# Optimization experiments

Hardware: AMD Instinct MI355X
Metric: run time of the kernel (lower is better)

Reference implementation:

```python
import jax, jax.numpy as jnp
import numpy as np

N, E, F_IN, H = 100000, 500000, 1433, 32


def setup_inputs() -> dict:
    key = jax.random.key(0)
    ks = jax.random.split(key, 8)
    return {
        "x": jax.random.normal(ks[0], (N, F_IN), jnp.float32),
        "edge_index": jax.random.randint(ks[1], (2, E), 0, N, dtype=jnp.int32),
        "W1l": jax.random.normal(ks[2], (H, F_IN), jnp.float32) * 0.02,
        "b1l": jnp.zeros((H,), jnp.float32),
        "W1r": jax.random.normal(ks[3], (H, F_IN), jnp.float32) * 0.02,
        "W2l": jax.random.normal(ks[4], (H, H), jnp.float32) * 0.1,
        "b2l": jnp.zeros((H,), jnp.float32),
        "W2r": jax.random.normal(ks[5], (H, H), jnp.float32) * 0.1,
    }


def _sage_conv(x, src, tgt, Wl, bl, Wr, n_nodes):
    # PyG SAGEConv (mean aggr): out = lin_l(mean_{j->i} x_j) + lin_r(x_i)
    msg_sum = jax.ops.segment_sum(x[src], tgt, num_segments=n_nodes)  # [N, d]
    cnt = jax.ops.segment_sum(jnp.ones((src.shape[0],), x.dtype), tgt,
                              num_segments=n_nodes)                  # [N]
    agg = msg_sum / jnp.maximum(cnt, 1.0)[:, None]  # isolated nodes -> 0
    return agg @ Wl.T + bl + x @ Wr.T


def reference(x, edge_index, W1l, b1l, W1r, W2l, b2l, W2r):
    src, tgt = edge_index[0], edge_index[1]
    n = x.shape[0]
    h = _sage_conv(x, src, tgt, W1l, b1l, W1r, n)   # [N, 32]
    h = _sage_conv(h, src, tgt, W2l, b2l, W2r, n)   # [N, 32]
    h = jax.nn.relu(h)
    # dropout is identity in eval mode (training=False)
    return jax.nn.log_softmax(h, axis=1)
```

## Files before the change

kernel.cpp:

```cpp
#include <hip/hip_runtime.h>
#include <hip/hip_bf16.h>


typedef __attribute__((ext_vector_type(8))) __bf16 bf16x8;
typedef __attribute__((ext_vector_type(4))) float f32x4;

constexpr int K1 = 1433;
constexpr int KP1 = 1536;
constexpr int BK = 32;
constexpr int NS = 45;
constexpr int BM = 128;

__device__ __forceinline__ void gload_lds16(const void* g, void* l) {
  __builtin_amdgcn_global_load_lds(
      reinterpret_cast<const __attribute__((address_space(1))) void*>(
          reinterpret_cast<uintptr_t>(g)),
      reinterpret_cast<__attribute__((address_space(3))) void*>(
          reinterpret_cast<uintptr_t>(l)),
      16, 0, 0);
}

__device__ __forceinline__ bf16x8 cvt8(const float4 lo, const float4 hi) {
  bf16x8 r;
  r[0] = (__bf16)lo.x; r[1] = (__bf16)lo.y;
  r[2] = (__bf16)lo.z; r[3] = (__bf16)lo.w;
  r[4] = (__bf16)hi.x; r[5] = (__bf16)hi.y;
  r[6] = (__bf16)hi.z; r[7] = (__bf16)hi.w;
  return r;
}

__global__ __launch_bounds__(256) void conv_w(const float* __restrict__ Wl,
                                              const float* __restrict__ Wr,
                                              __bf16* __restrict__ out, int K,
                                              int KP) {
  const int t = blockIdx.x * 256 + threadIdx.x;
  if (t >= 64 * KP) return;
  const int c = t / KP, k = t - c * KP;
  float v = 0.0f;
  if (k < K) v = (c < 32) ? Wl[(long)c * K + k] : Wr[(long)(c - 32) * K + k];
  out[t] = (__bf16)v;
}

__global__ __launch_bounds__(256) void gemm_big(const float* __restrict__ X,
                                                const __bf16* __restrict__ WB,
                                                float* __restrict__ Y,
                                                int Nrows) {
  __shared__ float ldsA[2][BM][BK];
  __shared__ __bf16 ldsB[2][64][BK];
  const int tid = threadIdx.x;
  const int w = tid >> 6, l = tid & 63;
  const int lr = l & 15, lg = l >> 4;
  const int row0 = blockIdx.x * BM;

  const int aRowIn = (l >> 3);
  const int aChunk = (l & 7) ^ aRowIn;
  long aRow[4];
#pragma unroll
  for (int i = 0; i < 4; ++i) {
    long r = (long)row0 + w * 32 + i * 8 + aRowIn;
    if (r >= Nrows) r = Nrows - 1;
    aRow[i] = r;
  }
  const float* const pAmax = X + (size_t)Nrows * K1 - 4;
  const int bRow = w * 16 + (l >> 2);
  const int bChunk = (l & 3) ^ ((l >> 3) & 3);
  const __bf16* const pB0 = WB + (long)bRow * KP1 + bChunk * 8;

  auto stage = [&](int s, int buf) {
    const int k0 = s * BK;
#pragma unroll
    for (int i = 0; i < 4; ++i) {
      const float* g = X + aRow[i] * K1 + k0 + aChunk * 4;
      if (g > pAmax) g = pAmax;
      gload_lds16(g, &ldsA[buf][w * 32 + i * 8][0]);
    }
    gload_lds16(pB0 + k0, &ldsB[buf][w * 16][0]);
  };

  f32x4 acc[2][4];
#pragma unroll
  for (int t = 0; t < 2; ++t)
#pragma unroll
    for (int j = 0; j < 4; ++j) acc[t][j] = (f32x4){0.f, 0.f, 0.f, 0.f};

  const int swzA = lr & 7;
  const int swzB = (lr >> 1) & 3;

  stage(0, 0);
#pragma unroll 1
  for (int s = 0; s < NS; ++s) {
    const int buf = s & 1;
    if (s + 1 < NS) {
      stage(s + 1, buf ^ 1);
      asm volatile("s_waitcnt vmcnt(5)" ::: "memory");
    } else {
      asm volatile("s_waitcnt vmcnt(0)" ::: "memory");
    }
    __builtin_amdgcn_s_barrier();
    __builtin_amdgcn_sched_barrier(0);
    bf16x8 bfrag[4];
#pragma unroll
    for (int ct = 0; ct < 4; ++ct) {
      const int br = ct * 16 + lr;
      bfrag[ct] = *reinterpret_cast<const bf16x8*>(
          &ldsB[buf][br][(lg ^ swzB) * 8]);
    }
#pragma unroll
    for (int t = 0; t < 2; ++t) {
      const int fr = w * 32 + t * 16 + lr;
      const float4 u = *reinterpret_cast<const float4*>(
          &ldsA[buf][fr][((lg * 2 + 0) ^ swzA) * 4]);
      const float4 v = *reinterpret_cast<const float4*>(
          &ldsA[buf][fr][((lg * 2 + 1) ^ swzA) * 4]);
      const bf16x8 af = cvt8(u, v);
#pragma unroll
      for (int ct = 0; ct < 4; ++ct)
        acc[t][ct] =
            __builtin_amdgcn_mfma_f32_16x16x32_bf16(af, bfrag[ct], acc[t][ct], 0, 0, 0);
    }
    __builtin_amdgcn_sched_barrier(0);
    __builtin_amdgcn_s_barrier();
  }

#pragma unroll
  for (int t = 0; t < 2; ++t) {
#pragma unroll
    for (int j = 0; j < 4; ++j) {
      const long R = (long)row0 + w * 32 + t * 16 + lg * 4 + j;
      if (R < Nrows) {
#pragma unroll
        for (int ct = 0; ct < 4; ++ct)
          Y[R * 64 + ct * 16 + lr] = acc[t][ct][j];
      }
    }
  }
}

__global__ __launch_bounds__(256) void gemm_small(const float* __restrict__ X,
                                                  const __bf16* __restrict__ WB,
                                                  float* __restrict__ Y,
                                                  int Nrows) {
  const int tid = threadIdx.x;
  const int w = tid >> 6, l = tid & 63;
  const int lr = l & 15, lg = l >> 4;
  const long rowbase = (long)blockIdx.x * 64 + (long)w * 16;
  long r0 = rowbase + lr;
  if (r0 >= Nrows) r0 = Nrows - 1;
  const float* px = X + r0 * 32 + lg * 8;
  const __bf16* pw = WB + lr * 32 + lg * 8;

  const float4 lo = *reinterpret_cast<const float4*>(px);
  const float4 hi = *reinterpret_cast<const float4*>(px + 4);
  const bf16x8 af = cvt8(lo, hi);
  f32x4 acc[4];
#pragma unroll
  for (int j = 0; j < 4; ++j) acc[j] = (f32x4){0.f, 0.f, 0.f, 0.f};
#pragma unroll
  for (int t = 0; t < 4; ++t) {
    const bf16x8 bf = *reinterpret_cast<const bf16x8*>(pw + t * 16 * 32);
    acc[t] = __builtin_amdgcn_mfma_f32_16x16x32_bf16(af, bf, acc[t], 0, 0, 0);
  }
#pragma unroll
  for (int j = 0; j < 4; ++j) {
    const long R = rowbase + lg * 4 + j;
    if (R < Nrows) {
#pragma unroll
      for (int ct = 0; ct < 4; ++ct) Y[R * 64 + ct * 16 + lr] = acc[ct][j];
    }
  }
}


__global__ __launch_bounds__(256) void hist_deg(const int* __restrict__ ei,
                                                int* __restrict__ deg, int E) {
  const int e = blockIdx.x * 256 + threadIdx.x;
  if (e < E) atomicAdd(&deg[ei[E + e]], 1);
}

__global__ __launch_bounds__(256) void scan_tilesum(const int* __restrict__ deg,
                                                    int* __restrict__ tileSum,
                                                    int n) {
  __shared__ int s[256];
  const int b = blockIdx.x, t = threadIdx.x;
  const int base = b * 2048 + t * 8;
  int v = 0;
#pragma unroll
  for (int j = 0; j < 8; ++j) {
    const int i = base + j;
    if (i < n) v += deg[i];
  }
  s[t] = v;
  __syncthreads();
  for (int d = 128; d > 0; d >>= 1) {
    if (t < d) s[t] += s[t + d];
    __syncthreads();
  }
  if (t == 0) tileSum[b] = s[0];
}

__global__ __launch_bounds__(64) void scan_tileoff(const int* __restrict__ tileSum,
                                                   int* __restrict__ tileOff,
                                                   int nT) {
  const int l = threadIdx.x;
  const int v = (l < nT) ? tileSum[l] : 0;
  int inc = v;
#pragma unroll
  for (int d = 1; d < 64; d <<= 1) {
    const int o = __shfl_up(inc, d);
    if (l >= d) inc += o;
  }
  if (l < nT) tileOff[l] = inc - v;
}

__global__ __launch_bounds__(256) void scan_offsets(const int* __restrict__ deg,
                                                    const int* __restrict__ tileOff,
                                                    int* __restrict__ off, int n) {
  __shared__ int warpTot[4];
  const int b = blockIdx.x, t = threadIdx.x;
  const int base = b * 2048 + t * 8;
  int v[8];
  int s = 0;
#pragma unroll
  for (int j = 0; j < 8; ++j) {
    const int i = base + j;
    v[j] = (i < n) ? deg[i] : 0;
    s += v[j];
  }
  const int l = t & 63, w = t >> 6;
  int inc = s;
#pragma unroll
  for (int d = 1; d < 64; d <<= 1) {
    const int o = __shfl_up(inc, d);
    if (l >= d) inc += o;
  }
  if (l == 63) warpTot[w] = inc;
  __syncthreads();
  int wo = 0;
  for (int k = 0; k < w; ++k) wo += warpTot[k];
  int ex = wo + (inc - s) + tileOff[b];
#pragma unroll
  for (int j = 0; j < 8; ++j) {
    const int i = base + j;
    if (i < n) {
      off[i] = ex;
      ex += v[j];
    }
  }
}

__global__ __launch_bounds__(256) void scatter_src(const int* __restrict__ ei,
                                                   const int* __restrict__ off,
                                                   int* __restrict__ fill,
                                                   int* __restrict__ ssrc,
                                                   int E) {
  const int e = blockIdx.x * 256 + threadIdx.x;
  if (e < E) {
    const int t = ei[E + e];
    const int p = off[t] + atomicAdd(&fill[t], 1);
    ssrc[p] = ei[e];
  }
}

template <int FINAL>
__global__ __launch_bounds__(256) void agg_fused(
    const int* __restrict__ off, const int* __restrict__ deg,
    const int* __restrict__ ssrc, const float* __restrict__ Y,
    const float* __restrict__ bias, float* __restrict__ out, int N) {
  const int t = blockIdx.x * 256 + threadIdx.x;
  const int i = t >> 5, c = t & 31;
  if (i >= N) return;
  const int st = off[i], d = deg[i];
  float acc = 0.0f;
  int e = 0;
  for (; e + 4 <= d; e += 4) {
    const int s0 = ssrc[st + e + 0];
    const int s1 = ssrc[st + e + 1];
    const int s2 = ssrc[st + e + 2];
    const int s3 = ssrc[st + e + 3];
    acc += Y[(long)s0 * 64 + c] + Y[(long)s1 * 64 + c] +
           Y[(long)s2 * 64 + c] + Y[(long)s3 * 64 + c];
  }
  for (; e < d; ++e) acc += Y[(long)ssrc[st + e] * 64 + c];
  const float mean = acc / fmaxf((float)d, 1.0f);
  float v = mean + bias[c] + Y[(long)i * 64 + 32 + c];
  if (FINAL) {
    v = fmaxf(v, 0.0f);
    float m = v;
#pragma unroll
    for (int dd = 16; dd >= 1; dd >>= 1) m = fmaxf(m, __shfl_xor(m, dd));
    const float ex = __expf(v - m);
    float s = ex;
#pragma unroll
    for (int dd = 16; dd >= 1; dd >>= 1) s += __shfl_xor(s, dd);
    out[(long)i * 32 + c] = (v - m) - __logf(s);
  } else {
    out[(long)i * 32 + c] = v;
  }
}

extern "C" void kernel_launch(void* const* d_in, const int* in_sizes, int n_in,
                              void* d_out, int out_size, void* d_ws,
                              size_t ws_size, hipStream_t stream) {
  const float* x = (const float*)d_in[0];
  const int* ei = (const int*)d_in[1];
  const float* W1l = (const float*)d_in[2];
  const float* b1l = (const float*)d_in[3];
  const float* W1r = (const float*)d_in[4];
  const float* W2l = (const float*)d_in[5];
  const float* b2l = (const float*)d_in[6];
  const float* W2r = (const float*)d_in[7];
  float* out = (float*)d_out;

  const int N = in_sizes[0] / K1;
  const int E = in_sizes[1] / 2;
  const int nTiles = (N + 2047) / 2048;

  char* ws = (char*)d_ws;
  size_t o = 0;
  auto alloc = [&](size_t bytes) {
    void* p = ws + o;
    o += (bytes + 255) & ~(size_t)255;
    return p;
  };
  float* ycomb = (float*)alloc((size_t)N * 64 * 4);
  float* h = (float*)alloc((size_t)N * 32 * 4);
  __bf16* wb1 = (__bf16*)alloc((size_t)64 * KP1 * 2);
  __bf16* wb2 = (__bf16*)alloc((size_t)64 * 32 * 2);
  int* deg = (int*)alloc((size_t)N * 4);
  int* off = (int*)alloc((size_t)N * 4);
  int* fill = (int*)alloc((size_t)N * 4);
  int* ssrc = (int*)alloc((size_t)E * 4);
  int* tileSum = (int*)alloc(64 * 4);
  int* tileOff = (int*)alloc(64 * 4);

  conv_w<<<(64 * KP1 + 255) / 256, 256, 0, stream>>>(W1l, W1r, wb1, K1, KP1);
  conv_w<<<(64 * 32 + 255) / 256, 256, 0, stream>>>(W2l, W2r, wb2, 32, 32);
  (void)hipMemsetAsync(deg, 0, (size_t)N * 4, stream);
  (void)hipMemsetAsync(fill, 0, (size_t)N * 4, stream);
  hist_deg<<<(E + 255) / 256, 256, 0, stream>>>(ei, deg, E);
  scan_tilesum<<<nTiles, 256, 0, stream>>>(deg, tileSum, N);
  scan_tileoff<<<1, 64, 0, stream>>>(tileSum, tileOff, nTiles);
  scan_offsets<<<nTiles, 256, 0, stream>>>(deg, tileOff, off, N);
  scatter_src<<<(E + 255) / 256, 256, 0, stream>>>(ei, off, fill, ssrc, E);

  gemm_big<<<(N + BM - 1) / BM, 256, 0, stream>>>(x, wb1, ycomb, N);
  agg_fused<0><<<(N * 32 + 255) / 256, 256, 0, stream>>>(off, deg, ssrc, ycomb,
                                                         b1l, h, N);
  gemm_small<<<(N + 63) / 64, 256, 0, stream>>>(h, wb2, ycomb, N);
  agg_fused<1><<<(N * 32 + 255) / 256, 256, 0, stream>>>(off, deg, ssrc, ycomb,
                                                         b2l, out, N);
}
```

Measured before the change: 300.8 us.

## Retile big GEMM to 32-row blocks with 256-deep K stages

Reorganizes the first-layer GEMM to use 32-row tiles with 256-wide K stages (6 stages instead of 45), each wave loading whole contiguous row segments and the four waves splitting the tile 2x2 over rows and output columns. Intended to cut per-stage barrier/loop overhead and improve load contiguity while raising block count. In exchange LDS use grows to about 128 KB per block, limiting occupancy to one block per CU, and the weight matrix is reloaded by four times as many blocks.

```diff
diff --git a/kernel.cpp b/kernel.cpp
--- a/kernel.cpp
+++ b/kernel.cpp
@@ -7,9 +7,9 @@
 
 constexpr int K1 = 1433;
 constexpr int KP1 = 1536;
-constexpr int BK = 32;
-constexpr int NS = 45;
-constexpr int BM = 128;
+constexpr int BK2 = 256;
+constexpr int NS2 = 6;
+constexpr int BM2 = 32;
 
 __device__ __forceinline__ void gload_lds16(const void* g, void* l) {
   __builtin_amdgcn_global_load_lds(
@@ -45,93 +45,91 @@
                                                 const __bf16* __restrict__ WB,
                                                 float* __restrict__ Y,
                                                 int Nrows) {
-  __shared__ float ldsA[2][BM][BK];
-  __shared__ __bf16 ldsB[2][64][BK];
+  __shared__ float ldsA[2][BM2][BK2];
+  __shared__ __bf16 ldsB[2][64][BK2];
   const int tid = threadIdx.x;
   const int w = tid >> 6, l = tid & 63;
   const int lr = l & 15, lg = l >> 4;
-  const int row0 = blockIdx.x * BM;
-
-  const int aRowIn = (l >> 3);
-  const int aChunk = (l & 7) ^ aRowIn;
-  long aRow[4];
-#pragma unroll
-  for (int i = 0; i < 4; ++i) {
-    long r = (long)row0 + w * 32 + i * 8 + aRowIn;
+  const int wr = w >> 1, wc = w & 1;
+  const int row0 = blockIdx.x * BM2;
+
+  const float* pA[8];
+#pragma unroll
+  for (int i = 0; i < 8; ++i) {
+    long r = (long)row0 + w * 8 + i;
     if (r >= Nrows) r = Nrows - 1;
-    aRow[i] = r;
+    pA[i] = X + r * (long)K1 + ((l ^ i) << 2);
   }
   const float* const pAmax = X + (size_t)Nrows * K1 - 4;
-  const int bRow = w * 16 + (l >> 2);
-  const int bChunk = (l & 3) ^ ((l >> 3) & 3);
-  const __bf16* const pB0 = WB + (long)bRow * KP1 + bChunk * 8;
+  const __bf16* pB[8];
+#pragma unroll
+  for (int j = 0; j < 8; ++j) {
+    const int J = w * 8 + j;
+    const int brow = 2 * J + (l >> 5);
+    pB[j] = WB + (long)brow * KP1 + (((l & 31) ^ (brow & 7)) << 3);
+  }
 
   auto stage = [&](int s, int buf) {
-    const int k0 = s * BK;
-#pragma unroll
-    for (int i = 0; i < 4; ++i) {
-      const float* g = X + aRow[i] * K1 + k0 + aChunk * 4;
+    const int k0 = s * BK2;
+#pragma unroll
+    for (int i = 0; i < 8; ++i) {
+      const float* g = pA[i] + k0;
       if (g > pAmax) g = pAmax;
-      gload_lds16(g, &ldsA[buf][w * 32 + i * 8][0]);
-    }
-    gload_lds16(pB0 + k0, &ldsB[buf][w * 16][0]);
+      gload_lds16(g, &ldsA[buf][w * 8 + i][0]);
+    }
+#pragma unroll
+    for (int j = 0; j < 8; ++j) {
+      gload_lds16(pB[j] + k0, &ldsB[buf][2 * (w * 8 + j)][0]);
+    }
   };
 
-  f32x4 acc[2][4];
-#pragma unroll
-  for (int t = 0; t < 2; ++t)
-#pragma unroll
-    for (int j = 0; j < 4; ++j) acc[t][j] = (f32x4){0.f, 0.f, 0.f, 0.f};
-
-  const int swzA = lr & 7;
-  const int swzB = (lr >> 1) & 3;
+  f32x4 acc[2];
+#pragma unroll
+  for (int ct = 0; ct < 2; ++ct) acc[ct] = (f32x4){0.f, 0.f, 0.f, 0.f};
+
+  const int swz = (lr & 7) << 4;
 
   stage(0, 0);
 #pragma unroll 1
-  for (int s = 0; s < NS; ++s) {
+  for (int s = 0; s < NS2; ++s) {
     const int buf = s & 1;
-    if (s + 1 < NS) {
+    if (s + 1 < NS2) {
       stage(s + 1, buf ^ 1);
-      asm volatile("s_waitcnt vmcnt(5)" ::: "memory");
+      asm volatile("s_waitcnt vmcnt(16)" ::: "memory");
     } else {
       asm volatile("s_waitcnt vmcnt(0)" ::: "memory");
     }
     __builtin_amdgcn_s_barrier();
     __builtin_amdgcn_sched_barrier(0);
-    bf16x8 bfrag[4];
-#pragma unroll
-    for (int ct = 0; ct < 4; ++ct) {
-      const int br = ct * 16 + lr;
-      bfrag[ct] = *reinterpret_cast<const bf16x8*>(
-          &ldsB[buf][br][(lg ^ swzB) * 8]);
-    }
-#pragma unroll
-    for (int t = 0; t < 2; ++t) {
-      const int fr = w * 32 + t * 16 + lr;
-      const float4 u = *reinterpret_cast<const float4*>(
-          &ldsA[buf][fr][((lg * 2 + 0) ^ swzA) * 4]);
-      const float4 v = *reinterpret_cast<const float4*>(
-          &ldsA[buf][fr][((lg * 2 + 1) ^ swzA) * 4]);
+#pragma unroll
+    for (int ks = 0; ks < 8; ++ks) {
+      const char* arow = (const char*)&ldsA[buf][wr * 16 + lr][0];
+      const int b0 = ks * 128 + lg * 32;
+      const float4 u = *reinterpret_cast<const float4*>(arow + (b0 ^ swz));
+      const float4 v =
+          *reinterpret_cast<const float4*>(arow + ((b0 + 16) ^ swz));
       const bf16x8 af = cvt8(u, v);
 #pragma unroll
-      for (int ct = 0; ct < 4; ++ct)
-        acc[t][ct] =
-            __builtin_amdgcn_mfma_f32_16x16x32_bf16(af, bfrag[ct], acc[t][ct], 0, 0, 0);
+      for (int ct = 0; ct < 2; ++ct) {
+        const char* bp =
+            (const char*)&ldsB[buf][wc * 32 + ct * 16 + lr][0];
+        const bf16x8 bf = *reinterpret_cast<const bf16x8*>(
+            bp + ((ks * 64 + lg * 16) ^ swz));
+        acc[ct] =
+            __builtin_amdgcn_mfma_f32_16x16x32_bf16(af, bf, acc[ct], 0, 0, 0);
+      }
     }
     __builtin_amdgcn_sched_barrier(0);
     __builtin_amdgcn_s_barrier();
   }
 
 #pragma unroll
-  for (int t = 0; t < 2; ++t) {
-#pragma unroll
-    for (int j = 0; j < 4; ++j) {
-      const long R = (long)row0 + w * 32 + t * 16 + lg * 4 + j;
-      if (R < Nrows) {
-#pragma unroll
-        for (int ct = 0; ct < 4; ++ct)
-          Y[R * 64 + ct * 16 + lr] = acc[t][ct][j];
-      }
+  for (int j = 0; j < 4; ++j) {
+    const long R = (long)row0 + wr * 16 + lg * 4 + j;
+    if (R < Nrows) {
+#pragma unroll
+      for (int ct = 0; ct < 2; ++ct)
+        Y[R * 64 + wc * 32 + ct * 16 + lr] = acc[ct][j];
     }
   }
 }
@@ -343,7 +341,7 @@
   scan_offsets<<<nTiles, 256, 0, stream>>>(deg, tileOff, off, N);
   scatter_src<<<(E + 255) / 256, 256, 0, stream>>>(ei, off, fill, ssrc, E);
 
-  gemm_big<<<(N + BM - 1) / BM, 256, 0, stream>>>(x, wb1, ycomb, N);
+  gemm_big<<<(N + BM2 - 1) / BM2, 256, 0, stream>>>(x, wb1, ycomb, N);
   agg_fused<0><<<(N * 32 + 255) / 256, 256, 0, stream>>>(off, deg, ssrc, ycomb,
                                                          b1l, h, N);
   gemm_small<<<(N + 63) / 64, 256, 0, stream>>>(h, wb2, ycomb, N);
```

Result: slower. 323.6 us (+7.6%).

## Fuse layer-1 aggregation with layer-2 GEMM and merge small setup kernels

Applied to the files above, without the earlier changes.

The first mean-aggregation now writes its 64-node tile of h as bf16 into shared memory, and the small 32x64 MFMA GEMM runs in the same kernel. This removes the h round trip through global memory and the separate gemm_small launch. The kernel also merges the two weight-conversion kernels, folds the tile-offset scan into scan_offsets, and clears deg and fill with a single memset, cutting several launches. In exchange each block processes its 8 nodes per row group serially, which may reduce the memory-level parallelism of the gather. A second Y buffer is also needed.

```diff
diff --git a/kernel.cpp b/kernel.cpp
--- a/kernel.cpp
+++ b/kernel.cpp
@@ -29,16 +29,27 @@
   return r;
 }
 
-__global__ __launch_bounds__(256) void conv_w(const float* __restrict__ Wl,
-                                              const float* __restrict__ Wr,
-                                              __bf16* __restrict__ out, int K,
-                                              int KP) {
+__global__ __launch_bounds__(256) void conv_w2(const float* __restrict__ W1l,
+                                               const float* __restrict__ W1r,
+                                               const float* __restrict__ W2l,
+                                               const float* __restrict__ W2r,
+                                               __bf16* __restrict__ wb1,
+                                               __bf16* __restrict__ wb2) {
   const int t = blockIdx.x * 256 + threadIdx.x;
-  if (t >= 64 * KP) return;
-  const int c = t / KP, k = t - c * KP;
-  float v = 0.0f;
-  if (k < K) v = (c < 32) ? Wl[(long)c * K + k] : Wr[(long)(c - 32) * K + k];
-  out[t] = (__bf16)v;
+  if (t < 64 * KP1) {
+    const int c = t / KP1, k = t - c * KP1;
+    float v = 0.0f;
+    if (k < K1)
+      v = (c < 32) ? W1l[(long)c * K1 + k] : W1r[(long)(c - 32) * K1 + k];
+    wb1[t] = (__bf16)v;
+  } else {
+    const int u = t - 64 * KP1;
+    if (u < 64 * 32) {
+      const int c = u >> 5, k = u & 31;
+      const float v = (c < 32) ? W2l[c * 32 + k] : W2r[(c - 32) * 32 + k];
+      wb2[u] = (__bf16)v;
+    }
+  }
 }
 
 __global__ __launch_bounds__(256) void gemm_big(const float* __restrict__ X,
@@ -136,40 +147,6 @@
   }
 }
 
-__global__ __launch_bounds__(256) void gemm_small(const float* __restrict__ X,
-                                                  const __bf16* __restrict__ WB,
-                                                  float* __restrict__ Y,
-                                                  int Nrows) {
-  const int tid = threadIdx.x;
-  const int w = tid >> 6, l = tid & 63;
-  const int lr = l & 15, lg = l >> 4;
-  const long rowbase = (long)blockIdx.x * 64 + (long)w * 16;
-  long r0 = rowbase + lr;
-  if (r0 >= Nrows) r0 = Nrows - 1;
-  const float* px = X + r0 * 32 + lg * 8;
-  const __bf16* pw = WB + lr * 32 + lg * 8;
-
-  const float4 lo = *reinterpret_cast<const float4*>(px);
-  const float4 hi = *reinterpret_cast<const float4*>(px + 4);
-  const bf16x8 af = cvt8(lo, hi);
-  f32x4 acc[4];
-#pragma unroll
-  for (int j = 0; j < 4; ++j) acc[j] = (f32x4){0.f, 0.f, 0.f, 0.f};
-#pragma unroll
-  for (int t = 0; t < 4; ++t) {
-    const bf16x8 bf = *reinterpret_cast<const bf16x8*>(pw + t * 16 * 32);
-    acc[t] = __builtin_amdgcn_mfma_f32_16x16x32_bf16(af, bf, acc[t], 0, 0, 0);
-  }
-#pragma unroll
-  for (int j = 0; j < 4; ++j) {
-    const long R = rowbase + lg * 4 + j;
-    if (R < Nrows) {
-#pragma unroll
-      for (int ct = 0; ct < 4; ++ct) Y[R * 64 + ct * 16 + lr] = acc[ct][j];
-    }
-  }
-}
-
 
 __global__ __launch_bounds__(256) void hist_deg(const int* __restrict__ ei,
                                                 int* __restrict__ deg, int E) {
@@ -198,25 +175,19 @@
   if (t == 0) tileSum[b] = s[0];
 }
 
-__global__ __launch_bounds__(64) void scan_tileoff(const int* __restrict__ tileSum,
-                                                   int* __restrict__ tileOff,
-                                                   int nT) {
-  const int l = threadIdx.x;
-  const int v = (l < nT) ? tileSum[l] : 0;
-  int inc = v;
-#pragma unroll
-  for (int d = 1; d < 64; d <<= 1) {
-    const int o = __shfl_up(inc, d);
-    if (l >= d) inc += o;
-  }
-  if (l < nT) tileOff[l] = inc - v;
-}
-
 __global__ __launch_bounds__(256) void scan_offsets(const int* __restrict__ deg,
-                                                    const int* __restrict__ tileOff,
-                                                    int* __restrict__ off, int n) {
+                                                    const int* __restrict__ tileSum,
+                                                    int* __restrict__ off,
+                                                    int n, int nT) {
   __shared__ int warpTot[4];
+  __shared__ int tileOffS;
   const int b = blockIdx.x, t = threadIdx.x;
+  if (t < 64) {
+    int v = (t < b && t < nT) ? tileSum[t] : 0;
+#pragma unroll
+    for (int d = 1; d < 64; d <<= 1) v += __shfl_xor(v, d);
+    if (t == 0) tileOffS = v;
+  }
   const int base = b * 2048 + t * 8;
   int v[8];
   int s = 0;
@@ -237,7 +208,7 @@
   __syncthreads();
   int wo = 0;
   for (int k = 0; k < w; ++k) wo += warpTot[k];
-  int ex = wo + (inc - s) + tileOff[b];
+  int ex = wo + (inc - s) + tileOffS;
 #pragma unroll
   for (int j = 0; j < 8; ++j) {
     const int i = base + j;
@@ -261,8 +232,69 @@
   }
 }
 
-template <int FINAL>
-__global__ __launch_bounds__(256) void agg_fused(
+__global__ __launch_bounds__(256) void agg_gemm2(
+    const int* __restrict__ off, const int* __restrict__ deg,
+    const int* __restrict__ ssrc, const float* __restrict__ Y,
+    const float* __restrict__ b1, const __bf16* __restrict__ WB2,
+    float* __restrict__ Y2, int N) {
+  __shared__ __bf16 hs[64][40];
+  const int tid = threadIdx.x;
+  const int nb0 = blockIdx.x * 64;
+  const int c = tid & 31, r8 = tid >> 5;
+
+  int stA[8], dgA[8];
+#pragma unroll
+  for (int j = 0; j < 8; ++j) {
+    const int i = nb0 + r8 * 8 + j;
+    stA[j] = (i < N) ? off[i] : 0;
+    dgA[j] = (i < N) ? deg[i] : 0;
+  }
+#pragma unroll 1
+  for (int j = 0; j < 8; ++j) {
+    const int i = nb0 + r8 * 8 + j;
+    float hv = 0.0f;
+    if (i < N) {
+      const int st = stA[j], d = dgA[j];
+      float acc = 0.0f;
+      int e = 0;
+      for (; e + 4 <= d; e += 4) {
+        const int s0 = ssrc[st + e + 0];
+        const int s1 = ssrc[st + e + 1];
+        const int s2 = ssrc[st + e + 2];
+        const int s3 = ssrc[st + e + 3];
+        acc += Y[(long)s0 * 64 + c] + Y[(long)s1 * 64 + c] +
+               Y[(long)s2 * 64 + c] + Y[(long)s3 * 64 + c];
+      }
+      for (; e < d; ++e) acc += Y[(long)ssrc[st + e] * 64 + c];
+      hv = acc / fmaxf((float)d, 1.0f) + b1[c] + Y[(long)i * 64 + 32 + c];
+    }
+    hs[r8 * 8 + j][c] = (__bf16)hv;
+  }
+  __syncthreads();
+
+  const int w = tid >> 6, l = tid & 63;
+  const int lr = l & 15, lg = l >> 4;
+  const bf16x8 af = *reinterpret_cast<const bf16x8*>(&hs[w * 16 + lr][lg * 8]);
+  f32x4 acc4[4];
+#pragma unroll
+  for (int j = 0; j < 4; ++j) acc4[j] = (f32x4){0.f, 0.f, 0.f, 0.f};
+#pragma unroll
+  for (int ct = 0; ct < 4; ++ct) {
+    const bf16x8 bf = *reinterpret_cast<const bf16x8*>(
+        WB2 + (ct * 16 + lr) * 32 + lg * 8);
+    acc4[ct] = __builtin_amdgcn_mfma_f32_16x16x32_bf16(af, bf, acc4[ct], 0, 0, 0);
+  }
+#pragma unroll
+  for (int j = 0; j < 4; ++j) {
+    const long R = (long)nb0 + w * 16 + lg * 4 + j;
+    if (R < N) {
+#pragma unroll
+      for (int ct = 0; ct < 4; ++ct) Y2[R * 64 + ct * 16 + lr] = acc4[ct][j];
+    }
+  }
+}
+
+__global__ __launch_bounds__(256) void agg_final(
     const int* __restrict__ off, const int* __restrict__ deg,
     const int* __restrict__ ssrc, const float* __restrict__ Y,
     const float* __restrict__ bias, float* __restrict__ out, int N) {
@@ -283,19 +315,15 @@
   for (; e < d; ++e) acc += Y[(long)ssrc[st + e] * 64 + c];
   const float mean = acc / fmaxf((float)d, 1.0f);
   float v = mean + bias[c] + Y[(long)i * 64 + 32 + c];
-  if (FINAL) {
-    v = fmaxf(v, 0.0f);
-    float m = v;
-#pragma unroll
-    for (int dd = 16; dd >= 1; dd >>= 1) m = fmaxf(m, __shfl_xor(m, dd));
-    const float ex = __expf(v - m);
-    float s = ex;
-#pragma unroll
-    for (int dd = 16; dd >= 1; dd >>= 1) s += __shfl_xor(s, dd);
-    out[(long)i * 32 + c] = (v - m) - __logf(s);
-  } else {
-    out[(long)i * 32 + c] = v;
-  }
+  v = fmaxf(v, 0.0f);
+  float m = v;
+#pragma unroll
+  for (int dd = 16; dd >= 1; dd >>= 1) m = fmaxf(m, __shfl_xor(m, dd));
+  const float ex = __expf(v - m);
+  float s = ex;
+#pragma unroll
+  for (int dd = 16; dd >= 1; dd >>= 1) s += __shfl_xor(s, dd);
+  out[(long)i * 32 + c] = (v - m) - __logf(s);
 }
 
 extern "C" void kernel_launch(void* const* d_in, const int* in_sizes, int n_in,
@@ -322,31 +350,27 @@
     o += (bytes + 255) & ~(size_t)255;
     return p;
   };
-  float* ycomb = (float*)alloc((size_t)N * 64 * 4);
-  float* h = (float*)alloc((size_t)N * 32 * 4);
+  float* ycomb1 = (float*)alloc((size_t)N * 64 * 4);
+  float* ycomb2 = (float*)alloc((size_t)N * 64 * 4);
   __bf16* wb1 = (__bf16*)alloc((size_t)64 * KP1 * 2);
   __bf16* wb2 = (__bf16*)alloc((size_t)64 * 32 * 2);
-  int* deg = (int*)alloc((size_t)N * 4);
+  int* deg = (int*)alloc((size_t)2 * N * 4);
+  int* fill = deg + N;
   int* off = (int*)alloc((size_t)N * 4);
-  int* fill = (int*)alloc((size_t)N * 4);
   int* ssrc = (int*)alloc((size_t)E * 4);
   int* tileSum = (int*)alloc(64 * 4);
-  int* tileOff = (int*)alloc(64 * 4);
-
-  conv_w<<<(64 * KP1 + 255) / 256, 256, 0, stream>>>(W1l, W1r, wb1, K1, KP1);
-  conv_w<<<(64 * 32 + 255) / 256, 256, 0, stream>>>(W2l, W2r, wb2, 32, 32);
-  (void)hipMemsetAsync(deg, 0, (size_t)N * 4, stream);
-  (void)hipMemsetAsync(fill, 0, (size_t)N * 4, stream);
+
+  conv_w2<<<(64 * KP1 + 64 * 32 + 255) / 256, 256, 0, stream>>>(
+      W1l, W1r, W2l, W2r, wb1, wb2);
+  (void)hipMemsetAsync(deg, 0, (size_t)2 * N * 4, stream);
   hist_deg<<<(E + 255) / 256, 256, 0, stream>>>(ei, deg, E);
   scan_tilesum<<<nTiles, 256, 0, stream>>>(deg, tileSum, N);
-  scan_tileoff<<<1, 64, 0, stream>>>(tileSum, tileOff, nTiles);
-  scan_offsets<<<nTiles, 256, 0, stream>>>(deg, tileOff, off, N);
+  scan_offsets<<<nTiles, 256, 0, stream>>>(deg, tileSum, off, N, nTiles);
   scatter_src<<<(E + 255) / 256, 256, 0, stream>>>(ei, off, fill, ssrc, E);
 
-  gemm_big<<<(N + BM - 1) / BM, 256, 0, stream>>>(x, wb1, ycomb, N);
-  agg_fused<0><<<(N * 32 + 255) / 256, 256, 0, stream>>>(off, deg, ssrc, ycomb,
-                                                         b1l, h, N);
-  gemm_small<<<(N + 63) / 64, 256, 0, stream>>>(h, wb2, ycomb, N);
-  agg_fused<1><<<(N * 32 + 255) / 256, 256, 0, stream>>>(off, deg, ssrc, ycomb,
-                                                         b2l, out, N);
-}
+  gemm_big<<<(N + BM - 1) / BM, 256, 0, stream>>>(x, wb1, ycomb1, N);
+  agg_gemm2<<<(N + 63) / 64, 256, 0, stream>>>(off, deg, ssrc, ycomb1, b1l,
+                                               wb2, ycomb2, N);
+  agg_final<<<(N * 32 + 255) / 256, 256, 0, stream>>>(off, deg, ssrc, ycomb2,
+                                                      b2l, out, N);
+}
```

Result: faster. 287.1 us (-4.6%).
